# Performance work log

Measured on AMD Instinct MI355X. Metric: run time of the kernel, lower is better.

## Reference

```python
import jax, jax.numpy as jnp
import numpy as np

N_NODES = 50000
N_EDGES = 800000
IN_NF = 64
OUT_NF = 64
HID = 128
H = 4
D = 64
HD = H * D
EDGE_IN = 2 * IN_NF + 1 + 6   # 135
MSG_IN = HID + 1 + 3 + 6      # 138


def _p(key, i, shape, scale=0.02):
    return scale * jax.random.normal(jax.random.fold_in(key, i), shape, dtype=jnp.float32)


def setup_inputs() -> dict:
    key = jax.random.key(0)
    ks = jax.random.split(key, 4)
    inp = {
        "h": jax.random.normal(ks[0], (N_NODES, IN_NF), dtype=jnp.float32),
        "x": jax.random.normal(ks[1], (N_NODES, 3), dtype=jnp.float32),
        "edge_index": jax.random.randint(ks[2], (2, N_EDGES), 0, N_NODES, dtype=jnp.int32),
        "mask": jnp.ones((N_EDGES,), dtype=bool),
    }
    pk = jax.random.fold_in(key, 7)
    i = iter(range(100))
    inp.update({
        "Wq": _p(pk, next(i), (IN_NF, HD)), "bq": jnp.zeros((HD,)),
        "Wk": _p(pk, next(i), (IN_NF, HD)), "bk": jnp.zeros((HD,)),
        "Wv": _p(pk, next(i), (IN_NF, HD)), "bv": jnp.zeros((HD,)),
        "Wo": _p(pk, next(i), (HD, OUT_NF)), "bo": jnp.zeros((OUT_NF,)),
        "pw1": _p(pk, next(i), (1, HID // 2)), "pb1": jnp.zeros((HID // 2,)),
        "pw2": _p(pk, next(i), (HID // 2, H)), "pb2": jnp.zeros((H,)),
        "ew1": _p(pk, next(i), (EDGE_IN, HID)), "eb1": jnp.zeros((HID,)),
        "ew2": _p(pk, next(i), (HID, HID)), "eb2": jnp.zeros((HID,)),
        "eww": _p(pk, next(i), (HID, H)), "ewb": jnp.zeros((H,)),
        "mw1": _p(pk, next(i), (MSG_IN, HID)), "mb1": jnp.zeros((HID,)),
        "mw2": _p(pk, next(i), (HID, HID)), "mb2": jnp.zeros((HID,)),
        "gw": _p(pk, next(i), (HID, H)), "gb": jnp.zeros((H,)),
        "cw1": _p(pk, next(i), (HID, HID)), "cb1": jnp.zeros((HID,)),
        "cw2": _p(pk, next(i), (HID, H)), "cb2": jnp.zeros((H,)),
        "coord_weights": jnp.ones((H,)),
        "xw1": _p(pk, next(i), (HID, HID)), "xb1": jnp.zeros((HID,)),
        "xw2": _p(pk, next(i), (HID, H)), "xb2": jnp.zeros((H,)),
    })
    return inp


def reference(h, x, edge_index, mask,
              Wq, bq, Wk, bk, Wv, bv, Wo, bo,
              pw1, pb1, pw2, pb2,
              ew1, eb1, ew2, eb2, eww, ewb,
              mw1, mb1, mw2, mb2,
              gw, gb, cw1, cb1, cw2, cb2,
              coord_weights, xw1, xb1, xw2, xb2):
    silu = jax.nn.silu
    row, col = edge_index[0], edge_index[1]
    n = h.shape[0]

    q = (h @ Wq + bq).reshape(n, H, D)
    k = (h @ Wk + bk).reshape(n, H, D)
    v = (h @ Wv + bv).reshape(n, H, D)

    rel_pos = x[row] - x[col]                         # [E,3]
    rel_dist = jnp.sum(rel_pos ** 2, -1, keepdims=True)  # [E,1]
    pos_enc = silu(rel_dist @ pw1 + pb1) @ pw2 + pb2     # [E,H]

    # torch .std() is unbiased (ddof=1)
    xn = (x - x.mean(0, keepdims=True)) / (jnp.std(x, 0, keepdims=True, ddof=1) + 1e-8)

    edge_attr = jnp.concatenate([h[row], h[col], rel_dist, xn[row], xn[col]], -1)
    ef = silu(edge_attr @ ew1 + eb1) @ ew2 + eb2      # [E,HID]
    ewt = ef @ eww + ewb                              # [E,H]

    attn = jnp.einsum('ehd,ehd->eh', q[row], k[col]) / jnp.sqrt(jnp.float32(D))
    attn = attn + pos_enc + ewt
    attn = jnp.where(mask[:, None], attn, jnp.float32(-1e9))

    amax = jax.ops.segment_max(attn, row, num_segments=n)   # [N,H]
    attn = jnp.exp(attn - amax[row])
    asum = jax.ops.segment_sum(attn, row, num_segments=n)
    attn = attn / (asum[row] + 1e-8)                         # [E,H]

    msg_in = jnp.concatenate([ef, attn.mean(1, keepdims=True), rel_pos, xn[row], xn[col]], -1)
    msgs = silu(msg_in @ mw1 + mb1) @ mw2 + mb2              # [E,HID]

    gates = jax.nn.sigmoid(msgs @ gw + gb)                   # [E,H]
    cwts = silu(msgs @ cw1 + cb1) @ cw2 + cb2                # [E,H]

    # per-head index_add into the same buffer == sum over heads of the scalar weight
    s = jnp.sum(gates * cwts * coord_weights, -1, keepdims=True)  # [E,1]
    base = 0.9 * rel_pos + 0.1 * x[col]
    coord_update = jax.ops.segment_sum(s * base / (n - 1), row, num_segments=n)

    cross_v = jnp.cross(rel_pos, jnp.roll(rel_pos, 1, axis=0))
    cg = silu(msgs @ xw1 + xb1) @ xw2 + xb2                  # [E,H]
    cross_s = jnp.sum(cg, -1, keepdims=True)
    coord_update = coord_update + jax.ops.segment_sum(cross_s * cross_v / (n - 1), row, num_segments=n)

    wv = jax.ops.segment_sum(attn[..., None] * v[col], row, num_segments=n)  # [N,H,D]
    out = wv.reshape(n, HD) @ Wo + bo
    return out, coord_update
```

## Files before the change

kernel.cpp:

```cpp
#include <hip/hip_runtime.h>
#include <hip/hip_bf16.h>

#define NN 50000
#define NE 800000

typedef __bf16 bf16x8 __attribute__((ext_vector_type(8)));
typedef float f4v __attribute__((ext_vector_type(4)));

__device__ __forceinline__ float silu_f(float v){
  return v*__builtin_amdgcn_rcpf(1.0f+__expf(-v));
}
__device__ __forceinline__ float bf2f(unsigned int u){ return __uint_as_float(u<<16); }
__device__ __forceinline__ unsigned bfr(float f){
  unsigned b = __float_as_uint(f);
  return b + 0x7fffu + ((b>>16)&1u);
}
__device__ __forceinline__ unsigned short f2bf(float f){ return (unsigned short)(bfr(f)>>16); }
__device__ __forceinline__ unsigned pk2(float a, float b){
  unsigned r;
  asm("v_cvt_pk_bf16_f32 %0, %1, %2" : "=v"(r) : "v"(a), "v"(b));
  return r;
}

union U8 { unsigned short us[8]; uint4 u4; };

__device__ __forceinline__ void pack8(unsigned short* dst, float4 a, float4 b){
  uint4 u;
  u.x = pk2(a.x,a.y); u.y = pk2(a.z,a.w);
  u.z = pk2(b.x,b.y); u.w = pk2(b.z,b.w);
  *(uint4*)dst = u;
}

__device__ __forceinline__ int lidx(int e, int c, int CH){
  return (e*CH + ((c & ~7) | ((c ^ e) & 7))) << 3;
}

template<int KC, int CH>
__device__ __forceinline__ void gemm_rm(const unsigned short* act, const unsigned short* wf,
                                        int wu, int lane, f4v (&acc)[4][2]){
  int le = lane & 15, quad = lane >> 4;
  #pragma unroll
  for (int kc=0;kc<KC;kc++){
    bf16x8 a0 = *(const bf16x8*)(wf + (((wu*2  )*KC + kc)<<9) + lane*8);
    bf16x8 a1 = *(const bf16x8*)(wf + (((wu*2+1)*KC + kc)<<9) + lane*8);
    int chunk = kc*4 + quad;
    #pragma unroll
    for (int et=0;et<4;et++){
      bf16x8 b = *(const bf16x8*)(act + lidx(et*16+le, chunk, CH));
      acc[et][0] = __builtin_amdgcn_mfma_f32_16x16x32_bf16(a0, b, acc[et][0], 0,0,0);
      acc[et][1] = __builtin_amdgcn_mfma_f32_16x16x32_bf16(a1, b, acc[et][1], 0,0,0);
    }
  }
}

template<int CH, bool SILU, bool BIAS>
__device__ __forceinline__ void epi_rm(unsigned short* dst, const f4v (&acc)[4][2],
                                       const float* bias, int wu, int lane){
  int le = lane & 15, quad = lane >> 4;
  #pragma unroll
  for (int ot=0; ot<2; ot++){
    float4 bv = make_float4(0,0,0,0);
    if (BIAS) bv = *(const float4*)(bias + wu*32 + ot*16 + quad*4);
    int chunk = wu*4 + ot*2 + (quad>>1);
    int soff = (quad&1)*4;
    #pragma unroll
    for (int et=0; et<4; et++){
      float v0=acc[et][ot][0], v1=acc[et][ot][1], v2=acc[et][ot][2], v3=acc[et][ot][3];
      if (BIAS){ v0+=bv.x; v1+=bv.y; v2+=bv.z; v3+=bv.w; }
      if (SILU){ v0=silu_f(v0); v1=silu_f(v1); v2=silu_f(v2); v3=silu_f(v3); }
      uint2 u; u.x = pk2(v0,v1); u.y = pk2(v2,v3);
      *(uint2*)(dst + lidx(et*16+le, chunk, CH) + soff) = u;
    }
  }
}

template<int CH>
__device__ __forceinline__ void mfma_head(const unsigned short* buf, const unsigned short* whf,
                                          int wu, int lane, float* dst ){
  int le = lane & 15, quad = lane >> 4;
  f4v hacc = {0.f,0.f,0.f,0.f};
  #pragma unroll
  for (int kc=0;kc<4;kc++){
    bf16x8 a = *(const bf16x8*)(whf + (kc<<9) + lane*8);
    bf16x8 b = *(const bf16x8*)(buf + lidx(wu*16+le, kc*4+quad, CH));
    hacc = __builtin_amdgcn_mfma_f32_16x16x32_bf16(a, b, hacc, 0,0,0);
  }
  if (quad==0){
    #pragma unroll
    for (int r=0;r<4;r++) dst[r*65 + wu*16 + le] = hacc[r];
  }
}

__global__ __launch_bounds__(256) void k_zero(float* __restrict__ p, int n){
  int i = blockIdx.x*256 + threadIdx.x;
  if (i < n) p[i] = 0.f;
}

__global__ __launch_bounds__(256) void k_wcomb(const float* __restrict__ ew2, const float* __restrict__ eww,
                                               const float* __restrict__ eb2, const float* __restrict__ ewb,
                                               const float* __restrict__ pb2,
                                               float* __restrict__ wcomb, float* __restrict__ stats){
  int t = threadIdx.x;
  #pragma unroll
  for (int o=t;o<512;o+=256){
    int i=o>>2, hh=o&3;
    float s=0.f;
    for (int j=0;j<128;j++) s += ew2[i*128+j]*eww[j*4+hh];
    wcomb[o]=s;
  }
  if (t<4){
    float s=0.f;
    for (int j=0;j<128;j++) s += eb2[j]*eww[j*4+t];
    stats[12+t] = s + ewb[t] + pb2[t];
  }
}

__global__ __launch_bounds__(256) void k_wprep(const float* __restrict__ src, unsigned short* __restrict__ dst,
                                               int Kreal, int KC){
  int idx = blockIdx.x*256 + threadIdx.x;
  int tot = 8*KC*512;
  if (idx >= tot) return;
  int nt  = idx/(KC*512); int rem = idx%(KC*512);
  int kc  = rem>>9;       int r2  = rem&511;
  int lq  = r2>>3;        int j   = r2&7;
  int k   = kc*32 + (lq>>4)*8 + j;
  int n   = nt*16 + (lq&15);
  float v = (k < Kreal) ? src[k*128 + n] : 0.f;
  dst[idx] = f2bf(v);
}

__global__ __launch_bounds__(256) void k_wprep4(const float* __restrict__ src, unsigned short* __restrict__ dst){
  int idx = blockIdx.x*256 + threadIdx.x;
  if (idx >= 2048) return;
  int kc = idx>>9; int r2 = idx&511; int lq = r2>>3; int j = r2&7;
  int k = kc*32 + (lq>>4)*8 + j;
  int n = lq&15;
  dst[idx] = f2bf((n<4) ? src[k*4+n] : 0.f);
}

__global__ __launch_bounds__(256) void k_stats(const float* __restrict__ x, float* __restrict__ stats){
  int i = blockIdx.x*256 + threadIdx.x;
  float v0=0.f,v1=0.f,v2=0.f;
  if (i < NN){ v0=x[i*3+0]; v1=x[i*3+1]; v2=x[i*3+2]; }
  float vals[6] = {v0,v1,v2,v0*v0,v1*v1,v2*v2};
  __shared__ float red[256];
  for (int c=0;c<6;c++){
    red[threadIdx.x]=vals[c];
    __syncthreads();
    for (int off=128; off>0; off>>=1){
      if (threadIdx.x < off) red[threadIdx.x] += red[threadIdx.x+off];
      __syncthreads();
    }
    if (threadIdx.x==0) atomicAdd(&stats[c], red[0]);
    __syncthreads();
  }
}

__global__ __launch_bounds__(64) void k_statsfin(float* __restrict__ stats){
  int t = threadIdx.x;
  if (t < 3){
    float s = stats[t], sq = stats[3+t];
    float mean = s/(float)NN;
    float var = (sq - s*s/(float)NN)/(float)(NN-1);
    float sd = sqrtf(var);
    stats[6+t] = mean;
    stats[9+t] = 1.0f/(sd + 1e-8f);
  }
}

__global__ __launch_bounds__(256) void k_qkv(const float* __restrict__ h,
    const float* __restrict__ Wq, const float* __restrict__ bq,
    const float* __restrict__ Wk, const float* __restrict__ bk,
    const float* __restrict__ Wv, const float* __restrict__ bv,
    unsigned short* __restrict__ q, unsigned short* __restrict__ kk, unsigned short* __restrict__ v){
  __shared__ float hs[32*68];
  int t = threadIdx.x;
  int by = blockIdx.y;
  int mat = by>>2; int quarter = by&3; int colbase = quarter*64;
  const float* W; const float* bb; unsigned short* outp;
  if (mat==0){W=Wq;bb=bq;outp=q;} else if (mat==1){W=Wk;bb=bk;outp=kk;} else {W=Wv;bb=bv;outp=v;}
  int r0 = blockIdx.x*32;
  {
    int rw = t>>3; int c0 = (t&7)*8;
    int row = r0 + rw;
    float4 a = make_float4(0,0,0,0), b2 = make_float4(0,0,0,0);
    if (row < NN){
      a  = *(const float4*)(h + (size_t)row*64 + c0);
      b2 = *(const float4*)(h + (size_t)row*64 + c0 + 4);
    }
    *(float4*)(&hs[rw*68 + c0])     = a;
    *(float4*)(&hs[rw*68 + c0 + 4]) = b2;
  }
  __syncthreads();
  int rg = t>>3; int cg = t&7; int col = colbase + cg*8;
  float acc[8];
  #pragma unroll
  for (int j=0;j<8;j++) acc[j]=0.f;
  for (int k2=0;k2<64;k2++){
    float a = hs[rg*68 + k2];
    const float4 w0 = *(const float4*)(W + k2*256 + col);
    const float4 w1 = *(const float4*)(W + k2*256 + col + 4);
    acc[0]+=a*w0.x; acc[1]+=a*w0.y; acc[2]+=a*w0.z; acc[3]+=a*w0.w;
    acc[4]+=a*w1.x; acc[5]+=a*w1.y; acc[6]+=a*w1.z; acc[7]+=a*w1.w;
  }
  int row = r0 + rg;
  if (row < NN){
    if (mat==2){
      #pragma unroll
      for (int j=0;j<8;j+=2){
        unsigned pu = pk2(acc[j]+bb[col+j], acc[j+1]+bb[col+j+1]);
        outp[(size_t)row*256 + (size_t)(cg*8+j)*4   + quarter] = (unsigned short)pu;
        outp[(size_t)row*256 + (size_t)(cg*8+j+1)*4 + quarter] = (unsigned short)(pu>>16);
      }
    } else {
      uint4 u;
      u.x = pk2(acc[0]+bb[col+0], acc[1]+bb[col+1]);
      u.y = pk2(acc[2]+bb[col+2], acc[3]+bb[col+3]);
      u.z = pk2(acc[4]+bb[col+4], acc[5]+bb[col+5]);
      u.w = pk2(acc[6]+bb[col+6], acc[7]+bb[col+7]);
      *(uint4*)(outp + (size_t)row*256 + col) = u;
    }
  }
}

__global__ __launch_bounds__(256) void k_count(const int* __restrict__ ei, int* __restrict__ counts){
  int e = blockIdx.x*256 + threadIdx.x;
  if (e < NE) atomicAdd(&counts[ei[e]], 1);
}

__global__ __launch_bounds__(256) void k_scan(int* __restrict__ counts, int* __restrict__ offs){
  __shared__ int ps[256];
  int t = threadIdx.x;
  int base = t*196;
  int s = 0;
  for (int i=0;i<196;i++){ int idx = base+i; if (idx < NN) s += counts[idx]; }
  ps[t]=s; __syncthreads();
  for (int off=1; off<256; off<<=1){
    int vv = (t>=off)? ps[t-off] : 0;
    __syncthreads();
    ps[t]+=vv;
    __syncthreads();
  }
  int run = ps[t]-s;
  for (int i=0;i<196;i++){
    int idx = base+i;
    if (idx < NN){ int c = counts[idx]; offs[idx]=run; counts[idx]=run; run+=c; }
  }
  if (t==255) offs[NN]=run;
}

__global__ __launch_bounds__(256) void k_fill(const int* __restrict__ ei, int* __restrict__ cursor, int* __restrict__ elist){
  int e = blockIdx.x*256 + threadIdx.x;
  if (e < NE){
    int r = ei[e];
    int p = atomicAdd(&cursor[r],1);
    elist[p] = e;
  }
}

__global__ __launch_bounds__(256) void k_e1(
    const float* __restrict__ h, const float* __restrict__ x, const int* __restrict__ ei,
    const float* __restrict__ stats,
    const unsigned short* __restrict__ qb, const unsigned short* __restrict__ kb,
    const unsigned short* __restrict__ wfrag, const unsigned short* __restrict__ whfrag,
    const float* __restrict__ eb1,
    const float* __restrict__ pw1, const float* __restrict__ pb1,
    const float* __restrict__ pw2,
    float* __restrict__ asum, float* __restrict__ eattn){
  __shared__ __align__(16) unsigned short bufIn[64*24*8];
  __shared__ float logit_s[256];
  __shared__ float ewt2_s[4*65];
  __shared__ float pos_s[4*65];
  __shared__ float rd_s[64], xnr_s[192], xnc_s[192];
  __shared__ int row_s[64], col_s[64];
  int t = threadIdx.x; int lane = t & 63; int w = t >> 6;
  int wu = __builtin_amdgcn_readfirstlane(w);
  int ebase = blockIdx.x * 64;

  for (int i=t;i<260;i+=256) pos_s[i]=0.f;
  if (t < 64){
    int ge = ebase + t;
    int r = ei[ge], c = ei[NE+ge];
    row_s[t]=r; col_s[t]=c;
    float xr0=x[r*3],xr1=x[r*3+1],xr2=x[r*3+2];
    float xc0=x[c*3],xc1=x[c*3+1],xc2=x[c*3+2];
    float rp0=xr0-xc0, rp1=xr1-xc1, rp2=xr2-xc2;
    rd_s[t]=rp0*rp0+rp1*rp1+rp2*rp2;
    float m0=stats[6],m1=stats[7],m2=stats[8],s0=stats[9],s1=stats[10],s2=stats[11];
    xnr_s[t*3+0]=(xr0-m0)*s0; xnr_s[t*3+1]=(xr1-m1)*s1; xnr_s[t*3+2]=(xr2-m2)*s2;
    xnc_s[t*3+0]=(xc0-m0)*s0; xnc_s[t*3+1]=(xc1-m1)*s1; xnc_s[t*3+2]=(xc2-m2)*s2;
  }
  __syncthreads();

  for (int ii=0; ii<16; ii++){
    int e = wu*16+ii;
    int r = row_s[e], c = col_s[e];
    uint2 qu = *(const uint2*)(qb + (size_t)r*256 + lane*4);
    uint2 ku = *(const uint2*)(kb + (size_t)c*256 + lane*4);
    float d = bf2f(qu.x&0xffffu)*bf2f(ku.x&0xffffu)
            + bf2f(qu.x>>16)   *bf2f(ku.x>>16)
            + bf2f(qu.y&0xffffu)*bf2f(ku.y&0xffffu)
            + bf2f(qu.y>>16)   *bf2f(ku.y>>16);
    d += __shfl_xor(d,1,16); d += __shfl_xor(d,2,16);
    d += __shfl_xor(d,4,16); d += __shfl_xor(d,8,16);
    if ((lane&15)==0) logit_s[e*4 + (lane>>4)] = d*0.125f;
  }
  {
    int jb = wu*16;
    float rd = rd_s[lane];
    float p0=0,p1=0,p2=0,p3=0;
    for (int j=jb; j<jb+16; j++){
      float hp = rd*pw1[j] + pb1[j];
      float hs = silu_f(hp);
      const float4 w4 = *(const float4*)(pw2 + j*4);
      p0+=hs*w4.x; p1+=hs*w4.y; p2+=hs*w4.z; p3+=hs*w4.w;
    }
    atomicAdd(&pos_s[0*65+lane],p0);
    atomicAdd(&pos_s[1*65+lane],p1);
    atomicAdd(&pos_s[2*65+lane],p2);
    atomicAdd(&pos_s[3*65+lane],p3);
  }
  {
    const float* hr = h + (size_t)row_s[lane]*64 + wu*16;
    pack8(&bufIn[lidx(lane, 2*wu,   24)], *(const float4*)(hr),   *(const float4*)(hr+4));
    pack8(&bufIn[lidx(lane, 2*wu+1, 24)], *(const float4*)(hr+8), *(const float4*)(hr+12));
    const float* hc = h + (size_t)col_s[lane]*64 + wu*16;
    pack8(&bufIn[lidx(lane, 8+2*wu, 24)], *(const float4*)(hc),   *(const float4*)(hc+4));
    pack8(&bufIn[lidx(lane, 9+2*wu, 24)], *(const float4*)(hc+8), *(const float4*)(hc+12));
  }
  if (t < 64){
    pack8(&bufIn[lidx(t,16,24)],
          make_float4(rd_s[t], xnr_s[t*3+0], xnr_s[t*3+1], xnr_s[t*3+2]),
          make_float4(xnc_s[t*3+0], xnc_s[t*3+1], xnc_s[t*3+2], 0.f));
  }
  {
    uint4 z4 = make_uint4(0,0,0,0);
    int e = t&63, j = t>>6;
    if (j < 3) *(uint4*)&bufIn[lidx(e, 17+j, 24)] = z4;
  }
  __syncthreads();
  f4v acc[4][2];
  f4v z = {0.f,0.f,0.f,0.f};
  #pragma unroll
  for (int et=0;et<4;et++){ acc[et][0]=z; acc[et][1]=z; }
  gemm_rm<5,24>(bufIn, wfrag + 0, wu, lane, acc);
  __syncthreads();
  epi_rm<24,true,true>(bufIn, acc, eb1, wu, lane);
  __syncthreads();
  mfma_head<24>(bufIn, whfrag + 0, wu, lane, ewt2_s);
  __syncthreads();
  {
    int e2 = t>>2, hh = t&3;
    float lg = logit_s[t] + stats[12+hh] + ewt2_s[hh*65+e2] + pos_s[hh*65+e2];
    float ex = __expf(lg);
    eattn[(size_t)ebase*4 + t] = ex;
    atomicAdd(&asum[row_s[e2]*4 + hh], ex);
  }
}

__global__ __launch_bounds__(256) void k_e2(
    const float* __restrict__ h, const float* __restrict__ x, const int* __restrict__ ei,
    const float* __restrict__ stats,
    const float* __restrict__ asum, const float* __restrict__ eattn,
    const unsigned short* __restrict__ wfrag, const unsigned short* __restrict__ whfrag,
    const float* __restrict__ eb1, const float* __restrict__ eb2,
    const float* __restrict__ mb1, const float* __restrict__ mb2,
    const float* __restrict__ gb,
    const float* __restrict__ cb1, const float* __restrict__ cb2,
    const float* __restrict__ coordw,
    const float* __restrict__ xb1, const float* __restrict__ xb2,
    float* __restrict__ cvec){
  __shared__ __align__(16) unsigned short bufIn[64*24*8];
  __shared__ __align__(16) unsigned short bufA [64*16*8];
  __shared__ float attn_s[256];
  __shared__ float g_s[4*65], c_s[4*65], xx_s[4*65];
  __shared__ float s_s[64], cs_s[64];
  __shared__ float rp_s[192], rd_s[64], xnr_s[192], xnc_s[192], xc_s[192];
  __shared__ int row_s[64], col_s[64];
  int t = threadIdx.x; int lane = t & 63; int w = t >> 6;
  int wu = __builtin_amdgcn_readfirstlane(w);
  int ebase = blockIdx.x * 64;

  if (t < 64){
    int ge = ebase + t;
    int r = ei[ge], c = ei[NE+ge];
    row_s[t]=r; col_s[t]=c;
    float xr0=x[r*3],xr1=x[r*3+1],xr2=x[r*3+2];
    float xc0=x[c*3],xc1=x[c*3+1],xc2=x[c*3+2];
    float rp0=xr0-xc0, rp1=xr1-xc1, rp2=xr2-xc2;
    rp_s[t*3+0]=rp0; rp_s[t*3+1]=rp1; rp_s[t*3+2]=rp2;
    rd_s[t]=rp0*rp0+rp1*rp1+rp2*rp2;
    xc_s[t*3+0]=xc0; xc_s[t*3+1]=xc1; xc_s[t*3+2]=xc2;
    float m0=stats[6],m1=stats[7],m2=stats[8],s0=stats[9],s1=stats[10],s2=stats[11];
    xnr_s[t*3+0]=(xr0-m0)*s0; xnr_s[t*3+1]=(xr1-m1)*s1; xnr_s[t*3+2]=(xr2-m2)*s2;
    xnc_s[t*3+0]=(xc0-m0)*s0; xnc_s[t*3+1]=(xc1-m1)*s1; xnc_s[t*3+2]=(xc2-m2)*s2;
  }
  __syncthreads();
  {
    int e2 = t>>2; int hh = t&3;
    float ex = eattn[(size_t)ebase*4 + t];
    float a = ex / (asum[row_s[e2]*4 + hh] + 1e-8f);
    attn_s[t]=a;
  }
  {
    const float* hr = h + (size_t)row_s[lane]*64 + wu*16;
    pack8(&bufIn[lidx(lane, 2*wu,   24)], *(const float4*)(hr),   *(const float4*)(hr+4));
    pack8(&bufIn[lidx(lane, 2*wu+1, 24)], *(const float4*)(hr+8), *(const float4*)(hr+12));
    const float* hc = h + (size_t)col_s[lane]*64 + wu*16;
    pack8(&bufIn[lidx(lane, 8+2*wu, 24)], *(const float4*)(hc),   *(const float4*)(hc+4));
    pack8(&bufIn[lidx(lane, 9+2*wu, 24)], *(const float4*)(hc+8), *(const float4*)(hc+12));
  }
  if (t < 64){
    pack8(&bufIn[lidx(t,16,24)],
          make_float4(rd_s[t], xnr_s[t*3+0], xnr_s[t*3+1], xnr_s[t*3+2]),
          make_float4(xnc_s[t*3+0], xnc_s[t*3+1], xnc_s[t*3+2], 0.f));
  }
  {
    uint4 z4 = make_uint4(0,0,0,0);
    int e = t&63, j = t>>6;
    *(uint4*)&bufIn[lidx(e, 17+j, 24)] = z4;
    if (j < 3) *(uint4*)&bufIn[lidx(e, 21+j, 24)] = z4;
  }
  __syncthreads();
  f4v acc[4][2];
  f4v z = {0.f,0.f,0.f,0.f};
  #pragma unroll
  for (int et=0;et<4;et++){ acc[et][0]=z; acc[et][1]=z; }
  gemm_rm<5,24>(bufIn, wfrag + 0, wu, lane, acc);
  epi_rm<16,true,true>(bufA, acc, eb1, wu, lane);
  __syncthreads();
  #pragma unroll
  for (int et=0;et<4;et++){ acc[et][0]=z; acc[et][1]=z; }
  gemm_rm<4,16>(bufA, wfrag + 20480, wu, lane, acc);
  epi_rm<24,false,true>(bufIn, acc, eb2, wu, lane);
  if (t < 64){
    float am = 0.25f*(attn_s[t*4]+attn_s[t*4+1]+attn_s[t*4+2]+attn_s[t*4+3]);
    pack8(&bufIn[lidx(t,16,24)],
          make_float4(am, rp_s[t*3+0], rp_s[t*3+1], rp_s[t*3+2]),
          make_float4(xnr_s[t*3+0], xnr_s[t*3+1], xnr_s[t*3+2], xnc_s[t*3+0]));
    pack8(&bufIn[lidx(t,17,24)],
          make_float4(xnc_s[t*3+1], xnc_s[t*3+2], 0.f, 0.f),
          make_float4(0.f,0.f,0.f,0.f));
  }
  __syncthreads();
  #pragma unroll
  for (int et=0;et<4;et++){ acc[et][0]=z; acc[et][1]=z; }
  gemm_rm<5,24>(bufIn, wfrag + 36864, wu, lane, acc);
  epi_rm<16,true,true>(bufA, acc, mb1, wu, lane);
  __syncthreads();
  #pragma unroll
  for (int et=0;et<4;et++){ acc[et][0]=z; acc[et][1]=z; }
  gemm_rm<4,16>(bufA, wfrag + 57344, wu, lane, acc);
  epi_rm<24,false,true>(bufIn, acc, mb2, wu, lane);
  __syncthreads();
  mfma_head<24>(bufIn, whfrag + 2048, wu, lane, g_s);
  f4v ax[4][2];
  #pragma unroll
  for (int et=0;et<4;et++){ acc[et][0]=z; acc[et][1]=z; ax[et][0]=z; ax[et][1]=z; }
  {
    const unsigned short* wfc = wfrag + 73728;
    const unsigned short* wfx = wfrag + 90112;
    int le = lane&15, quad = lane>>4;
    #pragma unroll
    for (int kc=0;kc<4;kc++){
      bf16x8 ac0 = *(const bf16x8*)(wfc + (((wu*2  )*4 + kc)<<9) + lane*8);
      bf16x8 ac1 = *(const bf16x8*)(wfc + (((wu*2+1)*4 + kc)<<9) + lane*8);
      bf16x8 ax0 = *(const bf16x8*)(wfx + (((wu*2  )*4 + kc)<<9) + lane*8);
      bf16x8 ax1 = *(const bf16x8*)(wfx + (((wu*2+1)*4 + kc)<<9) + lane*8);
      int chunk = kc*4 + quad;
      #pragma unroll
      for (int et=0;et<4;et++){
        bf16x8 b = *(const bf16x8*)(bufIn + lidx(et*16+le, chunk, 24));
        acc[et][0] = __builtin_amdgcn_mfma_f32_16x16x32_bf16(ac0, b, acc[et][0], 0,0,0);
        acc[et][1] = __builtin_amdgcn_mfma_f32_16x16x32_bf16(ac1, b, acc[et][1], 0,0,0);
        ax[et][0]  = __builtin_amdgcn_mfma_f32_16x16x32_bf16(ax0, b, ax[et][0], 0,0,0);
        ax[et][1]  = __builtin_amdgcn_mfma_f32_16x16x32_bf16(ax1, b, ax[et][1], 0,0,0);
      }
    }
  }
  __syncthreads();
  epi_rm<16,true,true>(bufA, acc, cb1, wu, lane);
  epi_rm<24,true,true>(bufIn, ax, xb1, wu, lane);
  __syncthreads();
  mfma_head<16>(bufA, whfrag + 4096, wu, lane, c_s);
  mfma_head<24>(bufIn, whfrag + 6144, wu, lane, xx_s);
  __syncthreads();
  {
    int e2 = t>>2; int hh = t&3;
    float g = __builtin_amdgcn_rcpf(1.0f+__expf(-(g_s[hh*65+e2]+gb[hh])));
    float cwv = c_s[hh*65+e2]+cb2[hh];
    float sv = g*cwv*coordw[hh];
    float csv = xx_s[hh*65+e2]+xb2[hh];
    sv += __shfl_xor(sv,1);  sv += __shfl_xor(sv,2);
    csv += __shfl_xor(csv,1); csv += __shfl_xor(csv,2);
    if (hh==0){ s_s[e2]=sv; cs_s[e2]=csv; }
  }
  __syncthreads();
  if (t < 64){
    int ge = ebase + t;
    float rp0=rp_s[t*3],rp1=rp_s[t*3+1],rp2=rp_s[t*3+2];
    float pp0,pp1,pp2;
    if (t > 0){ pp0=rp_s[(t-1)*3]; pp1=rp_s[(t-1)*3+1]; pp2=rp_s[(t-1)*3+2]; }
    else {
      int gp = (ebase==0)? (NE-1) : (ebase-1);
      int rr=ei[gp], cc2=ei[NE+gp];
      pp0=x[rr*3]-x[cc2*3]; pp1=x[rr*3+1]-x[cc2*3+1]; pp2=x[rr*3+2]-x[cc2*3+2];
    }
    float cv0 = rp1*pp2 - rp2*pp1;
    float cv1 = rp2*pp0 - rp0*pp2;
    float cv2 = rp0*pp1 - rp1*pp0;
    float sv = s_s[t], csv = cs_s[t];
    const float inv = 1.0f/49999.0f;
    cvec[(size_t)ge*3+0] = (sv*(0.9f*rp0+0.1f*xc_s[t*3+0]) + csv*cv0)*inv;
    cvec[(size_t)ge*3+1] = (sv*(0.9f*rp1+0.1f*xc_s[t*3+1]) + csv*cv1)*inv;
    cvec[(size_t)ge*3+2] = (sv*(0.9f*rp2+0.1f*xc_s[t*3+2]) + csv*cv2)*inv;
  }
}

__global__ __launch_bounds__(256) void k_aggout(
    const int* __restrict__ ei, const int* __restrict__ offs, const int* __restrict__ elist,
    const float* __restrict__ eattn, const unsigned short* __restrict__ vb,
    const float* __restrict__ cvec, const float* __restrict__ Wo, const float* __restrict__ bo,
    const float* __restrict__ asum,
    float* __restrict__ outp){
  __shared__ float wvs[4*256];
  int t = threadIdx.x; int lane = t & 63; int w = t >> 6;
  int node = blockIdx.x*4 + w;
  const int* colp = ei + NE;
  int s0 = offs[node], s1 = offs[node+1];
  float a0=0,a1=0,a2=0,a3=0,cc=0;
  int i = s0;
  for (; i+4<=s1; i+=4){
    int e0=elist[i], e1=elist[i+1], e2=elist[i+2], e3=elist[i+3];
    int c0=colp[e0], c1=colp[e1], c2=colp[e2], c3=colp[e3];
    uint2 v0 = *(const uint2*)(vb + (size_t)c0*256 + lane*4);
    uint2 v1 = *(const uint2*)(vb + (size_t)c1*256 + lane*4);
    uint2 v2 = *(const uint2*)(vb + (size_t)c2*256 + lane*4);
    uint2 v3 = *(const uint2*)(vb + (size_t)c3*256 + lane*4);
    float4 at0 = *(const float4*)(eattn + (size_t)e0*4);
    float4 at1 = *(const float4*)(eattn + (size_t)e1*4);
    float4 at2 = *(const float4*)(eattn + (size_t)e2*4);
    float4 at3 = *(const float4*)(eattn + (size_t)e3*4);
    if (lane < 3) cc += cvec[(size_t)e0*3+lane] + cvec[(size_t)e1*3+lane]
                      + cvec[(size_t)e2*3+lane] + cvec[(size_t)e3*3+lane];
    a0 += at0.x*bf2f(v0.x&0xffffu) + at1.x*bf2f(v1.x&0xffffu) + at2.x*bf2f(v2.x&0xffffu) + at3.x*bf2f(v3.x&0xffffu);
    a1 += at0.y*bf2f(v0.x>>16)     + at1.y*bf2f(v1.x>>16)     + at2.y*bf2f(v2.x>>16)     + at3.y*bf2f(v3.x>>16);
    a2 += at0.z*bf2f(v0.y&0xffffu) + at1.z*bf2f(v1.y&0xffffu) + at2.z*bf2f(v2.y&0xffffu) + at3.z*bf2f(v3.y&0xffffu);
    a3 += at0.w*bf2f(v0.y>>16)     + at1.w*bf2f(v1.y>>16)     + at2.w*bf2f(v2.y>>16)     + at3.w*bf2f(v3.y>>16);
  }
  for (; i<s1; i++){
    int e0 = elist[i];
    int c0 = colp[e0];
    uint2 v0 = *(const uint2*)(vb + (size_t)c0*256 + lane*4);
    float4 at0 = *(const float4*)(eattn + (size_t)e0*4);
    if (lane < 3) cc += cvec[(size_t)e0*3+lane];
    a0 += at0.x*bf2f(v0.x&0xffffu);
    a1 += at0.y*bf2f(v0.x>>16);
    a2 += at0.z*bf2f(v0.y&0xffffu);
    a3 += at0.w*bf2f(v0.y>>16);
  }
  {
    const float* as = asum + (size_t)node*4;
    a0 /= (as[0] + 1e-8f);
    a1 /= (as[1] + 1e-8f);
    a2 /= (as[2] + 1e-8f);
    a3 /= (as[3] + 1e-8f);
  }
  wvs[w*256 +       lane]=a0;
  wvs[w*256 +  64 + lane]=a1;
  wvs[w*256 + 128 + lane]=a2;
  wvs[w*256 + 192 + lane]=a3;
  if (lane < 3) outp[(size_t)NN*64 + (size_t)node*3 + lane] = cc;
  float o = bo[lane];
  #pragma unroll 4
  for (int k2=0;k2<256;k2++) o += wvs[w*256+k2] * Wo[k2*64+lane];
  outp[(size_t)node*64 + lane] = o;
}

extern "C" void kernel_launch(void* const* d_in, const int* in_sizes, int n_in,
                              void* d_out, int out_size, void* d_ws, size_t ws_size,
                              hipStream_t stream) {
  const float* h  = (const float*)d_in[0];
  const float* x  = (const float*)d_in[1];
  const int*   ei = (const int*)d_in[2];
  const float* Wq=(const float*)d_in[4];  const float* bq=(const float*)d_in[5];
  const float* Wk=(const float*)d_in[6];  const float* bk=(const float*)d_in[7];
  const float* Wv=(const float*)d_in[8];  const float* bv=(const float*)d_in[9];
  const float* Wo=(const float*)d_in[10]; const float* bo=(const float*)d_in[11];
  const float* pw1=(const float*)d_in[12]; const float* pb1=(const float*)d_in[13];
  const float* pw2=(const float*)d_in[14]; const float* pb2=(const float*)d_in[15];
  const float* ew1=(const float*)d_in[16]; const float* eb1=(const float*)d_in[17];
  const float* ew2=(const float*)d_in[18]; const float* eb2=(const float*)d_in[19];
  const float* eww=(const float*)d_in[20]; const float* ewb=(const float*)d_in[21];
  const float* mw1=(const float*)d_in[22]; const float* mb1=(const float*)d_in[23];
  const float* mw2=(const float*)d_in[24]; const float* mb2=(const float*)d_in[25];
  const float* gw=(const float*)d_in[26];  const float* gb=(const float*)d_in[27];
  const float* cw1=(const float*)d_in[28]; const float* cb1=(const float*)d_in[29];
  const float* cw2=(const float*)d_in[30]; const float* cb2=(const float*)d_in[31];
  const float* coordw=(const float*)d_in[32];
  const float* xw1=(const float*)d_in[33]; const float* xb1=(const float*)d_in[34];
  const float* xw2=(const float*)d_in[35]; const float* xb2=(const float*)d_in[36];

  char* B = (char*)d_ws;
  float* eattn = (float*)(B + 0);
  float* cvec  = (float*)(B + 12800000);
  float* stats = (float*)(B + 22400000);
  float* asum  = (float*)(B + 22400064);
  int* counts  = (int*)(B + 23200064);
  int* offs    = (int*)(B + 23400064);
  unsigned short* wfrag = (unsigned short*)(B + 23600080);
  int* elist   = (int*)(B + 23813088);
  unsigned short* qb = (unsigned short*)(B + 27013088);
  unsigned short* kb = (unsigned short*)(B + 52613088);
  unsigned short* vb = (unsigned short*)(B + 78213088);
  unsigned short* whfrag = (unsigned short*)(B + 103813088);
  float* wcomb = (float*)elist;

  k_zero<<<977,256,0,stream>>>(stats, 250016);
  k_wcomb<<<1,256,0,stream>>>(ew2, eww, eb2, ewb, pb2, wcomb, stats);
  k_wprep<<<80,256,0,stream>>>(ew1, wfrag + 0,     135, 5);
  k_wprep<<<64,256,0,stream>>>(ew2, wfrag + 20480, 128, 4);
  k_wprep<<<80,256,0,stream>>>(mw1, wfrag + 36864, 138, 5);
  k_wprep<<<64,256,0,stream>>>(mw2, wfrag + 57344, 128, 4);
  k_wprep<<<64,256,0,stream>>>(cw1, wfrag + 73728, 128, 4);
  k_wprep<<<64,256,0,stream>>>(xw1, wfrag + 90112, 128, 4);
  k_wprep4<<<8,256,0,stream>>>(wcomb, whfrag + 0);
  k_wprep4<<<8,256,0,stream>>>(gw,  whfrag + 2048);
  k_wprep4<<<8,256,0,stream>>>(cw2, whfrag + 4096);
  k_wprep4<<<8,256,0,stream>>>(xw2, whfrag + 6144);

  k_stats<<<196,256,0,stream>>>(x, stats);
  k_statsfin<<<1,64,0,stream>>>(stats);
  k_qkv<<<dim3(1563,12),256,0,stream>>>(h,Wq,bq,Wk,bk,Wv,bv,qb,kb,vb);
  k_count<<<3125,256,0,stream>>>(ei,counts);
  k_scan<<<1,256,0,stream>>>(counts,offs);
  k_fill<<<3125,256,0,stream>>>(ei,counts,elist);
  k_e1<<<12500,256,0,stream>>>(h,x,ei,stats,qb,kb,wfrag,whfrag,eb1,pw1,pb1,pw2,asum,eattn);
  k_e2<<<12500,256,0,stream>>>(h,x,ei,stats,asum,eattn,wfrag,whfrag,eb1,eb2,mb1,mb2,gb,cb1,cb2,coordw,xb1,xb2,cvec);
  k_aggout<<<12500,256,0,stream>>>(ei,offs,elist,eattn,vb,cvec,Wo,bo,asum,(float*)d_out);
}
```

Measured before the change: 1.464 ms.

## Compute QKV projection with bf16 MFMA using pre-packed weight fragments

Replaces the scalar FP32 QKV projection with a single fused kernel that stages h rows as bf16 in shared memory and runs 16x16x32 bf16 MFMA against weight fragments pre-packed by a new prep kernel into the eattn scratch buffer. One block now covers 64 rows across all three matrices, so h is read once instead of twelve times. The cost is bf16 rounding of the inputs and weights, plus reuse of the eattn buffer, which must not be written before k_qkv2 finishes.

```diff
diff --git a/kernel.cpp b/kernel.cpp
--- a/kernel.cpp
+++ b/kernel.cpp
@@ -129,6 +129,17 @@
   dst[idx] = f2bf(v);
 }
 
+__global__ __launch_bounds__(256) void k_wprepq(const float* __restrict__ src, unsigned short* __restrict__ dst){
+  int idx = blockIdx.x*256 + threadIdx.x;
+  if (idx >= 16384) return;
+  int nt  = idx>>10;  int rem = idx&1023;
+  int kc  = rem>>9;   int r2  = rem&511;
+  int lq  = r2>>3;    int j   = r2&7;
+  int k   = kc*32 + (lq>>4)*8 + j;
+  int n   = nt*16 + (lq&15);
+  dst[idx] = f2bf(src[k*256 + n]);
+}
+
 __global__ __launch_bounds__(256) void k_wprep4(const float* __restrict__ src, unsigned short* __restrict__ dst){
   int idx = blockIdx.x*256 + threadIdx.x;
   if (idx >= 2048) return;
@@ -168,57 +179,66 @@
   }
 }
 
-__global__ __launch_bounds__(256) void k_qkv(const float* __restrict__ h,
-    const float* __restrict__ Wq, const float* __restrict__ bq,
-    const float* __restrict__ Wk, const float* __restrict__ bk,
-    const float* __restrict__ Wv, const float* __restrict__ bv,
+__global__ __launch_bounds__(256) void k_qkv2(const float* __restrict__ h,
+    const unsigned short* __restrict__ wqf,
+    const float* __restrict__ bq, const float* __restrict__ bk, const float* __restrict__ bv,
     unsigned short* __restrict__ q, unsigned short* __restrict__ kk, unsigned short* __restrict__ v){
-  __shared__ float hs[32*68];
-  int t = threadIdx.x;
-  int by = blockIdx.y;
-  int mat = by>>2; int quarter = by&3; int colbase = quarter*64;
-  const float* W; const float* bb; unsigned short* outp;
-  if (mat==0){W=Wq;bb=bq;outp=q;} else if (mat==1){W=Wk;bb=bk;outp=kk;} else {W=Wv;bb=bv;outp=v;}
-  int r0 = blockIdx.x*32;
-  {
-    int rw = t>>3; int c0 = (t&7)*8;
-    int row = r0 + rw;
-    float4 a = make_float4(0,0,0,0), b2 = make_float4(0,0,0,0);
+  __shared__ __align__(16) unsigned short hstage[64*8*8];
+  int t = threadIdx.x; int lane = t & 63; int w = t >> 6;
+  int wu = __builtin_amdgcn_readfirstlane(w);
+  int r0 = blockIdx.x*64;
+  {
+    int row = r0 + lane;
+    float4 a = make_float4(0,0,0,0), b2 = make_float4(0,0,0,0),
+           c = make_float4(0,0,0,0), d2 = make_float4(0,0,0,0);
     if (row < NN){
-      a  = *(const float4*)(h + (size_t)row*64 + c0);
-      b2 = *(const float4*)(h + (size_t)row*64 + c0 + 4);
-    }
-    *(float4*)(&hs[rw*68 + c0])     = a;
-    *(float4*)(&hs[rw*68 + c0 + 4]) = b2;
-  }
-  __syncthreads();
-  int rg = t>>3; int cg = t&7; int col = colbase + cg*8;
-  float acc[8];
-  #pragma unroll
-  for (int j=0;j<8;j++) acc[j]=0.f;
-  for (int k2=0;k2<64;k2++){
-    float a = hs[rg*68 + k2];
-    const float4 w0 = *(const float4*)(W + k2*256 + col);
-    const float4 w1 = *(const float4*)(W + k2*256 + col + 4);
-    acc[0]+=a*w0.x; acc[1]+=a*w0.y; acc[2]+=a*w0.z; acc[3]+=a*w0.w;
-    acc[4]+=a*w1.x; acc[5]+=a*w1.y; acc[6]+=a*w1.z; acc[7]+=a*w1.w;
-  }
-  int row = r0 + rg;
-  if (row < NN){
-    if (mat==2){
+      const float* hr = h + (size_t)row*64 + wu*16;
+      a  = *(const float4*)(hr);    b2 = *(const float4*)(hr+4);
+      c  = *(const float4*)(hr+8);  d2 = *(const float4*)(hr+12);
+    }
+    pack8(&hstage[lidx(lane, 2*wu,   8)], a, b2);
+    pack8(&hstage[lidx(lane, 2*wu+1, 8)], c, d2);
+  }
+  __syncthreads();
+  int le = lane & 15, quad = lane >> 4;
+  #pragma unroll
+  for (int ti=0; ti<12; ti++){
+    int tt = ti*4 + wu;
+    f4v acc[4];
+    f4v z = {0.f,0.f,0.f,0.f};
+    acc[0]=z; acc[1]=z; acc[2]=z; acc[3]=z;
+    #pragma unroll
+    for (int kc=0;kc<2;kc++){
+      bf16x8 a = *(const bf16x8*)(wqf + ((tt*2 + kc)<<9) + lane*8);
+      int chunk = kc*4 + quad;
       #pragma unroll
-      for (int j=0;j<8;j+=2){
-        unsigned pu = pk2(acc[j]+bb[col+j], acc[j+1]+bb[col+j+1]);
-        outp[(size_t)row*256 + (size_t)(cg*8+j)*4   + quarter] = (unsigned short)pu;
-        outp[(size_t)row*256 + (size_t)(cg*8+j+1)*4 + quarter] = (unsigned short)(pu>>16);
+      for (int et=0;et<4;et++){
+        bf16x8 b = *(const bf16x8*)(hstage + lidx(et*16+le, chunk, 8));
+        acc[et] = __builtin_amdgcn_mfma_f32_16x16x32_bf16(a, b, acc[et], 0,0,0);
       }
-    } else {
-      uint4 u;
-      u.x = pk2(acc[0]+bb[col+0], acc[1]+bb[col+1]);
-      u.y = pk2(acc[2]+bb[col+2], acc[3]+bb[col+3]);
-      u.z = pk2(acc[4]+bb[col+4], acc[5]+bb[col+5]);
-      u.w = pk2(acc[6]+bb[col+6], acc[7]+bb[col+7]);
-      *(uint4*)(outp + (size_t)row*256 + col) = u;
+    }
+    int mat = tt>>4; int ct = tt&15;
+    const float* bias = (mat==0)? bq : (mat==1)? bk : bv;
+    unsigned short* outp = (mat==0)? q : (mat==1)? kk : v;
+    float4 bv4 = *(const float4*)(bias + ct*16 + quad*4);
+    int col = ct*16 + quad*4;
+    #pragma unroll
+    for (int et=0;et<4;et++){
+      int row2 = r0 + et*16 + le;
+      if (row2 < NN){
+        float v0=acc[et][0]+bv4.x, v1=acc[et][1]+bv4.y, v2=acc[et][2]+bv4.z, v3=acc[et][3]+bv4.w;
+        if (mat<2){
+          uint2 u; u.x = pk2(v0,v1); u.y = pk2(v2,v3);
+          *(uint2*)(outp + (size_t)row2*256 + col) = u;
+        } else {
+          int head = col>>6, dd = col&63;
+          unsigned short* vp = outp + (size_t)row2*256 + (size_t)dd*4 + head;
+          vp[0]  = f2bf(v0);
+          vp[4]  = f2bf(v1);
+          vp[8]  = f2bf(v2);
+          vp[12] = f2bf(v3);
+        }
+      }
     }
   }
 }
@@ -615,6 +635,7 @@
   unsigned short* vb = (unsigned short*)(B + 78213088);
   unsigned short* whfrag = (unsigned short*)(B + 103813088);
   float* wcomb = (float*)elist;
+  unsigned short* qkvf = (unsigned short*)eattn;
 
   k_zero<<<977,256,0,stream>>>(stats, 250016);
   k_wcomb<<<1,256,0,stream>>>(ew2, eww, eb2, ewb, pb2, wcomb, stats);
@@ -624,6 +645,9 @@
   k_wprep<<<64,256,0,stream>>>(mw2, wfrag + 57344, 128, 4);
   k_wprep<<<64,256,0,stream>>>(cw1, wfrag + 73728, 128, 4);
   k_wprep<<<64,256,0,stream>>>(xw1, wfrag + 90112, 128, 4);
+  k_wprepq<<<64,256,0,stream>>>(Wq, qkvf + 0);
+  k_wprepq<<<64,256,0,stream>>>(Wk, qkvf + 16384);
+  k_wprepq<<<64,256,0,stream>>>(Wv, qkvf + 32768);
   k_wprep4<<<8,256,0,stream>>>(wcomb, whfrag + 0);
   k_wprep4<<<8,256,0,stream>>>(gw,  whfrag + 2048);
   k_wprep4<<<8,256,0,stream>>>(cw2, whfrag + 4096);
@@ -631,7 +655,7 @@
 
   k_stats<<<196,256,0,stream>>>(x, stats);
   k_statsfin<<<1,64,0,stream>>>(stats);
-  k_qkv<<<dim3(1563,12),256,0,stream>>>(h,Wq,bq,Wk,bk,Wv,bv,qb,kb,vb);
+  k_qkv2<<<782,256,0,stream>>>(h, qkvf, bq, bk, bv, qb, kb, vb);
   k_count<<<3125,256,0,stream>>>(ei,counts);
   k_scan<<<1,256,0,stream>>>(counts,offs);
   k_fill<<<3125,256,0,stream>>>(ei,counts,elist);
```

Measured after the change: 1.237 ms. -15.5%, faster.
